# Kernel tuning notes

Measured on AMD Instinct MI355X. Metric: run time of the kernel, lower is better.

## Reference

```python
import jax, jax.numpy as jnp
import numpy as np

D = 64; B = 1024; M = 32; K = 16; L = 8
N_ENT = 200000; N_REL_VOCAB = 65; N_USERS = 100000; NKG = 65536
KG_WEIGHT = 1.0


def _normalize(x, eps=1e-12):
    n = jnp.sqrt(jnp.sum(x * x, axis=-1, keepdims=True))
    return x / jnp.maximum(n, eps)


def _forward(entity_emb, relation_emb, user_emb, gate, W_u_mlp, b_u_mlp, W_re,
             W_agg, b_agg, W_gatt, b_gatt, W_iatt, b_iatt, W_tatt, b_tatt,
             W_ih, W_hh, b_ih, b_hh,
             user_indices, ent_his_self, ent_his_nbr, rel_his,
             ent_pos_self, ent_pos_nbr, rel_pos,
             ent_neg_self, ent_neg_nbr, rel_neg,
             gb_his_self, gb_his_path, gb_pos_self, gb_pos_path,
             gb_neg_self, gb_neg_path, kg_head, kg_rel, kg_tail, kg_tail_neg):

    def gru_last(x):  # x: [N, L, D] -> final hidden [N, D] (PyTorch GRU gate order r,z,n)
        def step(h, xt):
            gi = xt @ W_ih.T + b_ih
            gh = h @ W_hh.T + b_hh
            ir, iz, in_ = jnp.split(gi, 3, axis=-1)
            hr, hz, hn = jnp.split(gh, 3, axis=-1)
            r = jax.nn.sigmoid(ir + hr)
            z = jax.nn.sigmoid(iz + hz)
            n = jnp.tanh(in_ + r * hn)
            return (1 - z) * n + z * h, None
        h0 = jnp.zeros((x.shape[0], D), x.dtype)
        hT, _ = jax.lax.scan(step, h0, jnp.swapaxes(x, 0, 1))
        return hT

    def agg_lc(self_idx, nbr_idx, rel_idx, u_em):
        # self_idx [N,1], nbr_idx/rel_idx [N,K], u_em [N,D]
        self_v = entity_emb[self_idx[:, 0]]                       # [N,D]
        nbr_v = entity_emb[nbr_idx]                               # [N,K,D]
        rel_v = relation_emb[rel_idx]                             # [N,K,D]
        nere = jnp.concatenate([nbr_v, rel_v], -1) @ W_re.T       # [N,K,D]
        u_att = jax.nn.relu(u_em @ W_tatt.T + b_tatt)             # [N,D]
        self1 = jnp.broadcast_to(self_v[:, None, :], nbr_v.shape)
        trans = jnp.tanh(jnp.concatenate([self1, nere], -1) @ W_gatt.T + b_gatt)
        att = jax.nn.softmax(jnp.sum(u_att[:, None, :] * trans, -1), axis=1)  # [N,K]
        new_v = jnp.einsum('nk,nkd->nd', att, nbr_v)
        agg = jnp.tanh(jnp.concatenate([self_v, new_v], -1) @ W_agg.T + b_agg)
        return self_v, _normalize(agg)

    def agg_gb(self_idx, path_idx):
        self_v = entity_emb[self_idx[:, 0]]
        hT = gru_last(entity_emb[path_idx])
        agg = jnp.tanh(jnp.concatenate([self_v, hT], -1) @ W_agg.T + b_agg)
        return _normalize(agg)

    def rs_att(hist, pre):  # hist [B,M,2D], pre [B,2D]
        pre_e = jnp.broadcast_to(pre[:, None, :], hist.shape)
        logits = jnp.tanh(jnp.concatenate([hist, pre_e], -1) @ W_iatt.T + b_iatt)[..., 0]
        att = jax.nn.softmax(logits, axis=1)
        return jnp.einsum('bm,bmd->bd', att, hist)

    user_g = user_emb[user_indices]                               # [B,D]
    g = jax.nn.sigmoid(gate)

    N = B * M
    u_rep = jnp.broadcast_to(user_g[:, None, :], (B, M, D)).reshape(N, D)
    self_hist, his_lc = agg_lc(ent_his_self.reshape(N, 1), ent_his_nbr.reshape(N, K),
                               rel_his.reshape(N, K), u_rep)
    his_gb = agg_gb(gb_his_self.reshape(N, 1), gb_his_path.reshape(N, L))
    item_hist = jnp.concatenate(
        [self_hist.reshape(B, M, D),
         (g * his_lc + (1 - g) * his_gb).reshape(B, M, D)], -1)   # [B,M,2D]

    def item_branch(self_idx, nbr_idx, rel_idx, gb_self, gb_path):
        self_v, lc = agg_lc(self_idx, nbr_idx, rel_idx, user_g)
        gb = agg_gb(gb_self, gb_path)
        item = jnp.concatenate([self_v, g * lc + (1 - g) * gb], -1)  # [B,2D]
        u_lc = rs_att(item_hist, item)                               # [B,2D]
        u = jax.nn.relu(jnp.concatenate([user_g, u_lc], -1) @ W_u_mlp.T + b_u_mlp)
        u = jnp.concatenate([user_g, _normalize(u)], -1)             # [B,2D]
        return jnp.sum(u * item, axis=1)

    pos_score = item_branch(ent_pos_self, ent_pos_nbr, rel_pos, gb_pos_self, gb_pos_path)
    neg_score = item_branch(ent_neg_self, ent_neg_nbr, rel_neg, gb_neg_self, gb_neg_path)
    rs_loss = -jnp.mean(jax.nn.log_sigmoid(pos_score - neg_score))

    head = entity_emb[kg_head]; rel = relation_emb[kg_rel]
    tail = entity_emb[kg_tail]; tail_ne = entity_emb[kg_tail_neg]
    nere = jnp.concatenate([tail, rel], 1) @ W_re.T
    nere_ne = jnp.concatenate([tail_ne, rel], 1) @ W_re.T
    s = jnp.sum((head - nere) ** 2, 1)
    s_ne = jnp.sum((head - nere_ne) ** 2, 1)
    kg_loss = -jnp.mean(jax.nn.log_sigmoid(s_ne - s))

    all_loss = rs_loss + KG_WEIGHT * kg_loss
    return pos_score, neg_score, all_loss


def setup_inputs() -> dict:
    key = jax.random.key(0)
    ks = iter(jax.random.split(key, 48))

    def nrm(shape, scale=0.1):
        return (scale * jax.random.normal(next(ks), shape)).astype(jnp.float32)

    def idx(shape, hi):
        return jax.random.randint(next(ks), shape, 0, hi)

    return dict(
        user_indices=idx((B,), N_USERS),
        ent_his_self=idx((B, M, 1), N_ENT),
        ent_his_nbr=idx((B, M, K), N_ENT),
        rel_his=idx((B, M, K), N_REL_VOCAB),
        ent_pos_self=idx((B, 1), N_ENT),
        ent_pos_nbr=idx((B, K), N_ENT),
        rel_pos=idx((B, K), N_REL_VOCAB),
        ent_neg_self=idx((B, 1), N_ENT),
        ent_neg_nbr=idx((B, K), N_ENT),
        rel_neg=idx((B, K), N_REL_VOCAB),
        gb_his_self=idx((B, M, 1), N_ENT),
        gb_his_path=idx((B, M, L), N_ENT),
        gb_pos_self=idx((B, 1), N_ENT),
        gb_pos_path=idx((B, L), N_ENT),
        gb_neg_self=idx((B, 1), N_ENT),
        gb_neg_path=idx((B, L), N_ENT),
        kg_head=idx((NKG,), N_ENT),
        kg_rel=idx((NKG,), N_REL_VOCAB),
        kg_tail=idx((NKG,), N_ENT),
        kg_tail_neg=idx((NKG,), N_ENT),
        entity_emb=nrm((N_ENT, D)),
        relation_emb=nrm((N_REL_VOCAB, D)),
        user_emb=nrm((N_USERS, D)),
        gate=jnp.zeros((D,), jnp.float32),
        W_u_mlp=nrm((D, 3 * D)), b_u_mlp=jnp.zeros((D,), jnp.float32),
        W_re=nrm((D, 2 * D)),
        W_agg=nrm((D, 2 * D)), b_agg=jnp.zeros((D,), jnp.float32),
        W_gatt=nrm((D, 2 * D)), b_gatt=jnp.zeros((D,), jnp.float32),
        W_iatt=nrm((1, 4 * D)), b_iatt=jnp.zeros((1,), jnp.float32),
        W_tatt=nrm((D, D)), b_tatt=jnp.zeros((D,), jnp.float32),
        W_ih=nrm((3 * D, D)), W_hh=nrm((3 * D, D)),
        b_ih=jnp.zeros((3 * D,), jnp.float32), b_hh=jnp.zeros((3 * D,), jnp.float32),
    )


def reference(user_indices, ent_his_self, ent_his_nbr, rel_his,
              ent_pos_self, ent_pos_nbr, rel_pos,
              ent_neg_self, ent_neg_nbr, rel_neg,
              gb_his_self, gb_his_path, gb_pos_self, gb_pos_path,
              gb_neg_self, gb_neg_path, kg_head, kg_rel, kg_tail, kg_tail_neg,
              entity_emb, relation_emb, user_emb, gate, W_u_mlp, b_u_mlp, W_re,
              W_agg, b_agg, W_gatt, b_gatt, W_iatt, b_iatt, W_tatt, b_tatt,
              W_ih, W_hh, b_ih, b_hh):
    return _forward(entity_emb, relation_emb, user_emb, gate, W_u_mlp, b_u_mlp, W_re,
                    W_agg, b_agg, W_gatt, b_gatt, W_iatt, b_iatt, W_tatt, b_tatt,
                    W_ih, W_hh, b_ih, b_hh,
                    user_indices, ent_his_self, ent_his_nbr, rel_his,
                    ent_pos_self, ent_pos_nbr, rel_pos,
                    ent_neg_self, ent_neg_nbr, rel_neg,
                    gb_his_self, gb_his_path, gb_pos_self, gb_pos_path,
                    gb_neg_self, gb_neg_path, kg_head, kg_rel, kg_tail, kg_tail_neg)
```

## Files before the change

### kernel.cpp

```cpp
#include <hip/hip_runtime.h>

#define DEV __device__ __forceinline__

#define Dd   64
#define Bb   1024
#define Mm   32
#define Kk   16
#define Ll   8
#define NKGk 65536
#define NH   32768
#define ROWS (NH + 2*Bb)

typedef float v2f __attribute__((ext_vector_type(2)));

#define OFF_WTATT   0
#define OFF_WGS     4096
#define OFF_WCOMB   8192
#define OFF_WRE     16384
#define OFF_WAGG    24576
#define OFF_WU      32768
#define OFF_GVEC    45056
#define OFF_USERG   45120
#define OFF_UATT    110656
#define OFF_SELFH   176192
#define OFF_HISLC   2273344
#define OFF_HISGB   4370496
#define OFF_SELFPN  6467648
#define OFF_LCPN    6598720
#define OFF_GBPN    6729792
#define OFF_ULCPN   6860864
#define OFF_KGSUM   7123008
#define OFF_KGS     7123012
#define OFF_WIHP    7123072
#define OFF_WHHP    7135360
#define OFF_WAGP    7147648
#define OFF_RELC    7155840
#define OFF_RELR    7160000

DEV float4 ld4(const float* p){ return *reinterpret_cast<const float4*>(p); }
DEV void st4(float* p, const float4 v){ *reinterpret_cast<float4*>(p) = v; }

DEV float tanh_fast(float x){
  float cx = fminf(15.f, fmaxf(-15.f, x));
  float e = __expf(2.f*cx);
  return __fdividef(e - 1.f, e + 1.f);
}
DEV float sigmoid_fast(float x){ return __fdividef(1.f, 1.f + __expf(-x)); }

#define MVJ(ACC_, WROW_, XS_) { \
  _Pragma("unroll") for (int d4_ = 0; d4_ < 16; ++d4_){ \
    float4 w_ = *(const float4*)((WROW_) + 4*d4_); \
    ACC_[4*d4_+0] += w_.x*(XS_); ACC_[4*d4_+1] += w_.y*(XS_); \
    ACC_[4*d4_+2] += w_.z*(XS_); ACC_[4*d4_+3] += w_.w*(XS_); } }

__global__ void prep1_kernel(const float* __restrict__ W_tatt, const float* __restrict__ W_gatt,
                             const float* __restrict__ W_re, const float* __restrict__ W_agg,
                             const float* __restrict__ W_u, const float* __restrict__ W_ih,
                             const float* __restrict__ W_hh, const float* __restrict__ gate,
                             float* __restrict__ ws)
{
  int g = blockIdx.x*256 + threadIdx.x;
  for (int i = g; i < 4096; i += 8192){
    int d = i >> 6, j = i & 63;
    ws[OFF_WTATT + j*64 + d] = W_tatt[i];
    ws[OFF_WGS   + j*64 + d] = W_gatt[d*128 + j];
  }
  for (int i = g; i < 8192; i += 8192){
    int j = i >> 6, d = i & 63;
    ws[OFF_WRE  + i] = W_re[d*128 + j];
    ws[OFF_WAGG + i] = W_agg[d*128 + j];
    float s = 0.f;
    for (int dp = 0; dp < 64; ++dp) s += W_gatt[d*128 + 64 + dp] * W_re[dp*128 + j];
    ws[OFF_WCOMB + i] = s;
  }
  for (int i = g; i < 12288; i += 8192){
    int j = i >> 6, d = i & 63;
    ws[OFF_WU + i] = W_u[d*192 + j];
  }
  for (int i = g; i < 12288; i += 8192){
    int jc = i / 768, r1 = i - jc*768;
    int ww = r1 / 96,  r2 = r1 - ww*96;
    int jj = r2 / 24,  r3 = r2 - jj*24;
    int gg = r3 >> 3,  oi = r3 & 7;
    int j = jc*4 + jj, o = gg*64 + ww*8 + oi;
    ws[OFF_WIHP + i] = W_ih[o*64 + j];
    ws[OFF_WHHP + i] = W_hh[o*64 + j];
  }
  for (int i = g; i < 8192; i += 8192){
    int jc = i >> 8, r1 = i & 255;
    int ww = r1 >> 5, r2 = r1 & 31;
    int jj = r2 >> 3, oi = r2 & 7;
    ws[OFF_WAGP + i] = W_agg[(ww*8 + oi)*128 + jc*4 + jj];
  }
  if (g < 64) ws[OFF_GVEC + g] = sigmoid_fast(gate[g]);
}

__global__ void prep2_kernel(const float* __restrict__ relation, float* __restrict__ ws)
{
  int i = blockIdx.x*256 + threadIdx.x;
  if (i >= 4160) return;
  int r = i >> 6, d = i & 63;
  const float* re = relation + r*64;
  float s1 = 0.f, s2 = 0.f;
  for (int j = 0; j < 64; ++j){
    s1 += ws[OFF_WCOMB + (64+j)*64 + d] * re[j];
    s2 += ws[OFF_WRE   + (64+j)*64 + d] * re[j];
  }
  ws[OFF_RELC + i] = s1;
  ws[OFF_RELR + i] = s2;
}

__global__ void user_prep_kernel(const int* __restrict__ uidx, const float* __restrict__ user_emb,
                                 const float* __restrict__ b_tatt, float* __restrict__ ws)
{
  int gid = blockIdx.x*256 + threadIdx.x;
  int b = gid >> 6, lane = gid & 63;
  long ui = uidx[b];
  float ugd = user_emb[ui*64 + lane];
  ws[OFF_USERG + b*64 + lane] = ugd;
  const float* WtT = ws + OFF_WTATT;
  float acc = b_tatt[lane];
  for (int j = 0; j < 64; ++j) acc += WtT[j*64 + lane] * __shfl(ugd, j);
  ws[OFF_UATT + b*64 + lane] = fmaxf(acc, 0.f);
}

#define GACC(AR_, AZ_, AN_, WP_, XS_) { \
  v2f xx_; xx_.x = (XS_); xx_.y = (XS_); \
  AR_[0] += (*(const v2f*)((WP_)+ 0))*xx_; AR_[1] += (*(const v2f*)((WP_)+ 2))*xx_; \
  AR_[2] += (*(const v2f*)((WP_)+ 4))*xx_; AR_[3] += (*(const v2f*)((WP_)+ 6))*xx_; \
  AZ_[0] += (*(const v2f*)((WP_)+ 8))*xx_; AZ_[1] += (*(const v2f*)((WP_)+10))*xx_; \
  AZ_[2] += (*(const v2f*)((WP_)+12))*xx_; AZ_[3] += (*(const v2f*)((WP_)+14))*xx_; \
  AN_[0] += (*(const v2f*)((WP_)+16))*xx_; AN_[1] += (*(const v2f*)((WP_)+18))*xx_; \
  AN_[2] += (*(const v2f*)((WP_)+20))*xx_; AN_[3] += (*(const v2f*)((WP_)+22))*xx_; }

#define AGACC(AG_, WP_, XS_) { \
  v2f xx_; xx_.x = (XS_); xx_.y = (XS_); \
  AG_[0] += (*(const v2f*)((WP_)+0))*xx_; AG_[1] += (*(const v2f*)((WP_)+2))*xx_; \
  AG_[2] += (*(const v2f*)((WP_)+4))*xx_; AG_[3] += (*(const v2f*)((WP_)+6))*xx_; }

__global__ __launch_bounds__(512, 4) void fused_kernel(
  const int* __restrict__ ghS, const int* __restrict__ ghP,
  const int* __restrict__ gpS, const int* __restrict__ gpP,
  const int* __restrict__ gnS, const int* __restrict__ gnP,
  const float* __restrict__ b_ih, const float* __restrict__ b_hh,
  const float* __restrict__ WIHP, const float* __restrict__ WHHP,
  const float* __restrict__ WAGP,
  float* __restrict__ outHis, float* __restrict__ outPN,
  const int* __restrict__ ahS, const int* __restrict__ ahN, const int* __restrict__ ahR,
  const int* __restrict__ apS, const int* __restrict__ apN, const int* __restrict__ apR,
  const int* __restrict__ anS, const int* __restrict__ anN, const int* __restrict__ anR,
  const float* __restrict__ b_gatt, const float* __restrict__ b_agg,
  const float* __restrict__ entity, float* __restrict__ ws)
{
  __shared__ float SH[8320];
  int tid = threadIdx.x;
  int bid = blockIdx.x;
  int rep = bid / 3, pos = bid - rep*3;

  if (pos == 0){
    float (*hb)[65] = (float(*)[65])SH;
    float (*xb)[65] = (float(*)[65])(SH + 4160);
    int w = __builtin_amdgcn_readfirstlane(tid >> 6);
    int lane = tid & 63;
    int rbase = rep*64;
    const int *sIv, *pIv; float* aO; int nb0;
    if (rbase < NH)          { sIv=ghS; pIv=ghP; aO=outHis;       nb0=rbase; }
    else if (rbase < NH+Bb)  { sIv=gpS; pIv=gpP; aO=outPN;        nb0=rbase-NH; }
    else                     { sIv=gnS; pIv=gnP; aO=outPN+65536;  nb0=rbase-NH-Bb; }
    int o0 = w*8;
    int nrow = nb0 + lane;

    int pt = pIv[nrow*8];
    int pt_next = pIv[nrow*8 + 1];
    {
      const float* ex = entity + (long)pt*64 + o0;
      float4 xa0 = ld4(ex), xc0 = ld4(ex + 4);
      st4(&xb[lane][o0], xa0);
      st4(&xb[lane][o0+4], xc0);
    }
    __syncthreads();

    #pragma unroll 1
    for (int t = 0; t < 8; ++t){
      float4 xa = {0,0,0,0}, xc = {0,0,0,0};
      if (t < 7){
        const float* ex = entity + (long)pt_next*64 + o0;
        xa = ld4(ex); xc = ld4(ex + 4);
        if (t < 6) pt_next = pIv[nrow*8 + t + 2];
      }
      v2f ar[4], az[4], ah[4];
      #pragma unroll
      for (int p = 0; p < 4; ++p){
        ar[p].x = b_ih[o0+2*p]      + b_hh[o0+2*p];
        ar[p].y = b_ih[o0+2*p+1]    + b_hh[o0+2*p+1];
        az[p].x = b_ih[64+o0+2*p]   + b_hh[64+o0+2*p];
        az[p].y = b_ih[64+o0+2*p+1] + b_hh[64+o0+2*p+1];
        ah[p].x = b_hh[128+o0+2*p];   ah[p].y = b_hh[128+o0+2*p+1];
      }
      if (t){
        #pragma unroll 2
        for (int jc = 0; jc < 16; ++jc){
          const float* wp = WHHP + (jc*8 + w)*96;
          float4 h4 = ld4(&hb[lane][4*jc]);
          GACC(ar, az, ah, wp,      h4.x);
          GACC(ar, az, ah, wp + 24, h4.y);
          GACC(ar, az, ah, wp + 48, h4.z);
          GACC(ar, az, ah, wp + 72, h4.w);
        }
      }
      v2f an[4];
      #pragma unroll
      for (int p = 0; p < 4; ++p){ an[p].x = b_ih[128+o0+2*p]; an[p].y = b_ih[128+o0+2*p+1]; }
      #pragma unroll 2
      for (int jc = 0; jc < 16; ++jc){
        const float* wp = WIHP + (jc*8 + w)*96;
        float4 x4 = ld4(&xb[lane][4*jc]);
        GACC(ar, az, an, wp,      x4.x);
        GACC(ar, az, an, wp + 24, x4.y);
        GACC(ar, az, an, wp + 48, x4.z);
        GACC(ar, az, an, wp + 72, x4.w);
      }
      float hp[8] = {0,0,0,0,0,0,0,0};
      if (t){
        float4 hv0 = ld4(&hb[lane][o0]); float4 hv1 = ld4(&hb[lane][o0+4]);
        hp[0]=hv0.x; hp[1]=hv0.y; hp[2]=hv0.z; hp[3]=hv0.w;
        hp[4]=hv1.x; hp[5]=hv1.y; hp[6]=hv1.z; hp[7]=hv1.w;
      }
      float hn[8];
      #pragma unroll
      for (int p = 0; p < 4; ++p){
        float r0 = sigmoid_fast(ar[p].x), r1 = sigmoid_fast(ar[p].y);
        float z0 = sigmoid_fast(az[p].x), z1 = sigmoid_fast(az[p].y);
        float n0 = tanh_fast(an[p].x + r0*ah[p].x);
        float n1 = tanh_fast(an[p].y + r1*ah[p].y);
        hn[2*p]   = (1.f - z0)*n0 + z0*hp[2*p];
        hn[2*p+1] = (1.f - z1)*n1 + z1*hp[2*p+1];
      }
      __syncthreads();
      float4 s0 = {hn[0],hn[1],hn[2],hn[3]}, s1 = {hn[4],hn[5],hn[6],hn[7]};
      st4(&hb[lane][o0], s0);
      st4(&hb[lane][o0+4], s1);
      if (t < 7){
        st4(&xb[lane][o0], xa);
        st4(&xb[lane][o0+4], xc);
      }
      __syncthreads();
    }

    long si = sIv[nrow];
    const float* es = entity + si*64 + o0;
    float4 aa = ld4(es), cc = ld4(es + 4);
    v2f ag[4];
    #pragma unroll
    for (int p = 0; p < 4; ++p){ ag[p].x = b_agg[o0+2*p]; ag[p].y = b_agg[o0+2*p+1]; }
    #pragma unroll 2
    for (int jc = 0; jc < 16; ++jc){
      const float* wp = WAGP + ((16+jc)*8 + w)*32;
      float4 h4 = ld4(&hb[lane][4*jc]);
      AGACC(ag, wp,      h4.x);
      AGACC(ag, wp + 8,  h4.y);
      AGACC(ag, wp + 16, h4.z);
      AGACC(ag, wp + 24, h4.w);
    }
    st4(&xb[lane][o0], aa);
    st4(&xb[lane][o0+4], cc);
    __syncthreads();
    #pragma unroll 2
    for (int jc = 0; jc < 16; ++jc){
      const float* wp = WAGP + (jc*8 + w)*32;
      float4 x4 = ld4(&xb[lane][4*jc]);
      AGACC(ag, wp,      x4.x);
      AGACC(ag, wp + 8,  x4.y);
      AGACC(ag, wp + 16, x4.z);
      AGACC(ag, wp + 24, x4.w);
    }
    {
      float4 s0 = {tanh_fast(ag[0].x), tanh_fast(ag[0].y), tanh_fast(ag[1].x), tanh_fast(ag[1].y)};
      float4 s1 = {tanh_fast(ag[2].x), tanh_fast(ag[2].y), tanh_fast(ag[3].x), tanh_fast(ag[3].y)};
      st4(&hb[lane][o0], s0);
      st4(&hb[lane][o0+4], s1);
    }
    __syncthreads();
    int q = tid & 7, r = tid >> 3;
    float4 v0 = ld4(&hb[r][q*8]);
    float4 v1 = ld4(&hb[r][q*8+4]);
    float ss = v0.x*v0.x + v0.y*v0.y + v0.z*v0.z + v0.w*v0.w
             + v1.x*v1.x + v1.y*v1.y + v1.z*v1.z + v1.w*v1.w;
    ss += __shfl_xor(ss, 1); ss += __shfl_xor(ss, 2); ss += __shfl_xor(ss, 4);
    float rn = __fdividef(1.f, fmaxf(sqrtf(ss), 1e-12f));
    int n2 = nb0 + r;
    float4 o4a = {v0.x*rn, v0.y*rn, v0.z*rn, v0.w*rn};
    float4 o4b = {v1.x*rn, v1.y*rn, v1.z*rn, v1.w*rn};
    st4(aO + (long)n2*64 + q*8,     o4a);
    st4(aO + (long)n2*64 + q*8 + 4, o4b);
    return;
  }

  float* WL = SH;
  int ablk = rep*2 + (pos - 1);
  int tid2 = tid & 255;
  int sub  = tid >> 8;
  int k = tid2 & 15, rl = tid2 >> 4;
  int rbase = ablk*32;
  const int *sI, *nI, *rI; float *sO, *aO; int nb0, uhis;
  if (rbase < NH)          { sI=ahS; nI=ahN; rI=ahR; sO=ws+OFF_SELFH;        aO=ws+OFF_HISLC;       nb0=rbase;        uhis=1; }
  else if (rbase < NH+Bb)  { sI=apS; nI=apN; rI=apR; sO=ws+OFF_SELFPN;       aO=ws+OFF_LCPN;       nb0=rbase-NH;     uhis=0; }
  else                     { sI=anS; nI=anN; rI=anR; sO=ws+OFF_SELFPN+65536; aO=ws+OFF_LCPN+65536; nb0=rbase-NH-Bb;  uhis=0; }
  int n = nb0 + sub*16 + rl;
  int urow = uhis ? (n >> 5) : n;

  for (int i = tid; i < 1024; i += 512){
    st4(&WL[4*i],        ld4(ws + OFF_WCOMB + 4*i));
    st4(&WL[4096 + 4*i], ld4(ws + OFF_WGS   + 4*i));
  }

  const float* es = entity + (long)sI[n]*64;
  long nbI = nI[n*16 + k], rlI = rI[n*16 + k];
  const float* en = entity + nbI*64;

  float acc[64];
  {
    const float* rt = ws + OFF_RELC + rlI*64;
    #pragma unroll
    for (int j4 = 0; j4 < 16; ++j4){
      float4 v = ld4(rt + 4*j4);
      acc[4*j4+0] = v.x; acc[4*j4+1] = v.y; acc[4*j4+2] = v.z; acc[4*j4+3] = v.w;
    }
  }
  __syncthreads();

  float4 sc4 = ld4(b_gatt + k*4);
  #pragma unroll 2
  for (int j4 = 0; j4 < 16; ++j4){
    float4 s4 = ld4(es + 4*j4);
    float4 w0 = *(const float4*)&WL[4096 + (4*j4+0)*64 + k*4];
    float4 w1 = *(const float4*)&WL[4096 + (4*j4+1)*64 + k*4];
    float4 w2 = *(const float4*)&WL[4096 + (4*j4+2)*64 + k*4];
    float4 w3 = *(const float4*)&WL[4096 + (4*j4+3)*64 + k*4];
    sc4.x += w0.x*s4.x + w1.x*s4.y + w2.x*s4.z + w3.x*s4.w;
    sc4.y += w0.y*s4.x + w1.y*s4.y + w2.y*s4.z + w3.y*s4.w;
    sc4.z += w0.z*s4.x + w1.z*s4.y + w2.z*s4.z + w3.z*s4.w;
    sc4.w += w0.w*s4.x + w1.w*s4.y + w2.w*s4.z + w3.w*s4.w;
  }
  st4(sO + (long)n*64 + k*4, ld4(es + k*4));

  {
    float4 x4 = ld4(en);
    #pragma unroll 2
    for (int j4 = 0; j4 < 16; ++j4){
      float4 xn = ld4(en + 4*((j4+1) & 15));
      MVJ(acc, &WL[(4*j4+0)*64], x4.x);
      MVJ(acc, &WL[(4*j4+1)*64], x4.y);
      MVJ(acc, &WL[(4*j4+2)*64], x4.z);
      MVJ(acc, &WL[(4*j4+3)*64], x4.w);
      x4 = xn;
    }
  }

  int gl = (tid & 63) & 48;
  const float* up = ws + OFF_UATT + (long)urow*64;
  float lg = 0.f;
  #pragma unroll
  for (int j4 = 0; j4 < 16; ++j4){
    float4 u4 = ld4(up + 4*j4);
    float s0 = __shfl(sc4.x, gl + j4);
    float s1 = __shfl(sc4.y, gl + j4);
    float s2 = __shfl(sc4.z, gl + j4);
    float s3 = __shfl(sc4.w, gl + j4);
    lg += u4.x*tanh_fast(acc[4*j4+0] + s0);
    lg += u4.y*tanh_fast(acc[4*j4+1] + s1);
    lg += u4.z*tanh_fast(acc[4*j4+2] + s2);
    lg += u4.w*tanh_fast(acc[4*j4+3] + s3);
  }
  float mx = lg;
  mx = fmaxf(mx, __shfl_xor(mx, 1)); mx = fmaxf(mx, __shfl_xor(mx, 2));
  mx = fmaxf(mx, __shfl_xor(mx, 4)); mx = fmaxf(mx, __shfl_xor(mx, 8));
  float e = __expf(lg - mx);
  float se = e;
  se += __shfl_xor(se, 1); se += __shfl_xor(se, 2);
  se += __shfl_xor(se, 4); se += __shfl_xor(se, 8);
  float att = __fdividef(e, se);

  __syncthreads();
  for (int i = tid; i < 2048; i += 512)
    st4(&WL[4*i], ld4(ws + OFF_WAGG + 4*i));
  __syncthreads();

  float4 a4 = ld4(b_agg + k*4);
  #pragma unroll 2
  for (int j4 = 0; j4 < 16; ++j4){
    float4 s4 = ld4(es + 4*j4);
    float4 w0 = *(const float4*)&WL[(4*j4+0)*64 + k*4];
    float4 w1 = *(const float4*)&WL[(4*j4+1)*64 + k*4];
    float4 w2 = *(const float4*)&WL[(4*j4+2)*64 + k*4];
    float4 w3 = *(const float4*)&WL[(4*j4+3)*64 + k*4];
    a4.x += w0.x*s4.x + w1.x*s4.y + w2.x*s4.z + w3.x*s4.w;
    a4.y += w0.y*s4.x + w1.y*s4.y + w2.y*s4.z + w3.y*s4.w;
    a4.z += w0.z*s4.x + w1.z*s4.y + w2.z*s4.z + w3.z*s4.w;
    a4.w += w0.w*s4.x + w1.w*s4.y + w2.w*s4.z + w3.w*s4.w;
  }
  #pragma unroll 2
  for (int j4 = 0; j4 < 16; ++j4){
    float4 x4 = ld4(en + 4*j4);
    float xs[4] = {x4.x, x4.y, x4.z, x4.w};
    #pragma unroll
    for (int jj = 0; jj < 4; ++jj){
      float v = att * xs[jj];
      v += __shfl_xor(v, 1); v += __shfl_xor(v, 2);
      v += __shfl_xor(v, 4); v += __shfl_xor(v, 8);
      float4 wv = *(const float4*)&WL[(64 + 4*j4 + jj)*64 + k*4];
      a4.x += wv.x*v; a4.y += wv.y*v; a4.z += wv.z*v; a4.w += wv.w*v;
    }
  }
  float t0 = tanh_fast(a4.x), t1 = tanh_fast(a4.y), t2 = tanh_fast(a4.z), t3 = tanh_fast(a4.w);
  float ss = t0*t0 + t1*t1 + t2*t2 + t3*t3;
  ss += __shfl_xor(ss, 1); ss += __shfl_xor(ss, 2);
  ss += __shfl_xor(ss, 4); ss += __shfl_xor(ss, 8);
  float rn = __fdividef(1.f, fmaxf(sqrtf(ss), 1e-12f));
  float4 o4; o4.x = t0*rn; o4.y = t1*rn; o4.z = t2*rn; o4.w = t3*rn;
  st4(aO + (long)n*64 + k*4, o4);
}

__global__ __launch_bounds__(512, 4) void fused2_kernel(
  const int* __restrict__ kh, const int* __restrict__ kr,
  const int* __restrict__ kt, const int* __restrict__ ktn,
  const float* __restrict__ W_iatt, const float* __restrict__ b_iatt,
  const float* __restrict__ b_u,
  const float* __restrict__ entity, const float* __restrict__ relation,
  float* __restrict__ ws, float* __restrict__ out)
{
  __shared__ float WL[4096];
  int tid = threadIdx.x;
  int bid = blockIdx.x;
  int type = bid & 1, rep = bid >> 1;

  if (type == 0){
    int idx = rep*512 + tid;
    int br = idx >> 16, r = idx & 65535;
    const int* tailI = br ? ktn : kt;
    for (int i = tid; i < 1024; i += 512)
      st4(&WL[4*i], ld4(ws + OFF_WRE + 4*i));

    long rel = kr[r];
    const float* et = entity + (long)tailI[r]*64;
    float acc[64];
    {
      const float* rt = ws + OFF_RELR + rel*64;
      #pragma unroll
      for (int j4 = 0; j4 < 16; ++j4){
        float4 v = ld4(rt + 4*j4);
        acc[4*j4+0] = v.x; acc[4*j4+1] = v.y; acc[4*j4+2] = v.z; acc[4*j4+3] = v.w;
      }
    }
    __syncthreads();
    {
      float4 x4 = ld4(et);
      #pragma unroll 2
      for (int j4 = 0; j4 < 16; ++j4){
        float4 xn = ld4(et + 4*((j4+1) & 15));
        MVJ(acc, &WL[(4*j4+0)*64], x4.x);
        MVJ(acc, &WL[(4*j4+1)*64], x4.y);
        MVJ(acc, &WL[(4*j4+2)*64], x4.z);
        MVJ(acc, &WL[(4*j4+3)*64], x4.w);
        x4 = xn;
      }
    }
    const float* eh = entity + (long)kh[r]*64;
    float s = 0.f;
    #pragma unroll
    for (int j4 = 0; j4 < 16; ++j4){
      float4 h4 = ld4(eh + 4*j4);
      float d0 = h4.x - acc[4*j4+0], d1 = h4.y - acc[4*j4+1];
      float d2 = h4.z - acc[4*j4+2], d3 = h4.w - acc[4*j4+3];
      s += d0*d0 + d1*d1 + d2*d2 + d3*d3;
    }
    ws[OFF_KGS + br*65536 + r] = s;
    return;
  }

  int gw = rep*8 + (tid >> 6), lane = tid & 63;
  int b = gw >> 1, br = gw & 1;
  const float* selfB = ws + OFF_SELFPN + br*65536 + b*64;
  const float* lcB   = ws + OFF_LCPN   + br*65536 + b*64;
  const float* gbB   = ws + OFF_GBPN   + br*65536 + b*64;
  const float* gvec  = ws + OFF_GVEC;
  const float* selfH = ws + OFF_SELFH;
  const float* hisLC = ws + OFF_HISLC;
  const float* hisGB = ws + OFF_HISGB;

  float gd = gvec[lane];
  float ugd = ws[OFF_USERG + b*64 + lane];
  float sv = selfB[lane], lcv = lcB[lane], gbv = gbB[lane];
  float gated = gd*lcv + (1.f - gd)*gbv;
  float part = W_iatt[128+lane]*sv + W_iatt[192+lane]*gated;
  #pragma unroll
  for (int m2 = 1; m2 < 64; m2 <<= 1) part += __shfl_xor(part, m2);
  float itemdot = part + b_iatt[0];

  int m = lane & 31, half = lane >> 5;
  long nrow = (long)(b*32 + m)*64;
  float sh = 0.f;
  if (half == 0){
    for (int j4 = 0; j4 < 16; ++j4){
      float4 h4 = ld4(selfH + nrow + 4*j4);
      float4 w4 = ld4(W_iatt + 4*j4);
      sh += w4.x*h4.x + w4.y*h4.y + w4.z*h4.z + w4.w*h4.w;
    }
  } else {
    for (int j4 = 0; j4 < 16; ++j4){
      float4 l4 = ld4(hisLC + nrow + 4*j4);
      float4 g4 = ld4(hisGB + nrow + 4*j4);
      float4 gg = ld4(gvec + 4*j4);
      float4 w4 = ld4(W_iatt + 64 + 4*j4);
      sh += w4.x*(gg.x*l4.x + (1.f-gg.x)*g4.x);
      sh += w4.y*(gg.y*l4.y + (1.f-gg.y)*g4.y);
      sh += w4.z*(gg.z*l4.z + (1.f-gg.z)*g4.z);
      sh += w4.w*(gg.w*l4.w + (1.f-gg.w)*g4.w);
    }
  }
  sh += __shfl_xor(sh, 32);
  float logit = tanh_fast(sh + itemdot);
  float mxv = logit;
  #pragma unroll
  for (int m2 = 1; m2 < 32; m2 <<= 1) mxv = fmaxf(mxv, __shfl_xor(mxv, m2));
  float e = __expf(logit - mxv);
  float se = e;
  #pragma unroll
  for (int m2 = 1; m2 < 32; m2 <<= 1) se += __shfl_xor(se, m2);
  float att = __fdividef(e, se);

  float u1 = 0.f, u2 = 0.f;
  for (int mm = 0; mm < 32; ++mm){
    float a = __shfl(att, mm);
    long nr = (long)(b*32 + mm)*64;
    float x1 = selfH[nr + lane];
    float x2 = gd*hisLC[nr + lane] + (1.f - gd)*hisGB[nr + lane];
    u1 += a*x1; u2 += a*x2;
  }

  const float* WuT = ws + OFF_WU;
  float acc = b_u[lane];
  for (int j = 0; j < 64; ++j) acc += WuT[j*64 + lane]        * __shfl(ugd, j);
  for (int j = 0; j < 64; ++j) acc += WuT[(64 + j)*64 + lane] * __shfl(u1, j);
  for (int j = 0; j < 64; ++j) acc += WuT[(128 + j)*64 + lane]* __shfl(u2, j);
  float uo = fmaxf(acc, 0.f);
  float ssv = uo*uo;
  #pragma unroll
  for (int m2 = 1; m2 < 64; m2 <<= 1) ssv += __shfl_xor(ssv, m2);
  float rn = __fdividef(1.f, fmaxf(sqrtf(ssv), 1e-12f));
  float nuo = uo*rn;
  float p = ugd*sv + nuo*gated;
  #pragma unroll
  for (int m2 = 1; m2 < 64; m2 <<= 1) p += __shfl_xor(p, m2);
  if (lane == 0) out[br*1024 + b] = p;
}

__global__ void kg_reduce_kernel(float* __restrict__ ws)
{
  int r = blockIdx.x*256 + threadIdx.x;
  float s  = ws[OFF_KGS + r];
  float sn = ws[OFF_KGS + 65536 + r];
  float dif = sn - s;
  float ls = fminf(dif, 0.f) - __logf(1.f + __expf(-fabsf(dif)));
  #pragma unroll
  for (int m2 = 1; m2 < 64; m2 <<= 1) ls += __shfl_xor(ls, m2);
  if ((threadIdx.x & 63) == 0) atomicAdd(ws + OFF_KGSUM, ls);
}

__global__ void loss_kernel(const float* __restrict__ ws, float* __restrict__ out)
{
  __shared__ float red[16];
  int t = threadIdx.x;
  float ps = out[t], ns_ = out[1024 + t];
  float dif = ps - ns_;
  float v = fminf(dif, 0.f) - __logf(1.f + __expf(-fabsf(dif)));
  #pragma unroll
  for (int m2 = 1; m2 < 64; m2 <<= 1) v += __shfl_xor(v, m2);
  if ((t & 63) == 0) red[t >> 6] = v;
  __syncthreads();
  if (t == 0){
    float s = 0.f;
    for (int i = 0; i < 16; ++i) s += red[i];
    float rs = -s * (1.f/1024.f);
    float kg = -ws[OFF_KGSUM] * (1.f/65536.f);
    out[2048] = rs + kg;
  }
}

extern "C" void kernel_launch(void* const* d_in, const int* in_sizes, int n_in,
                              void* d_out, int out_size, void* d_ws, size_t ws_size,
                              hipStream_t stream)
{
  const int* user_indices = (const int*)d_in[0];
  const int* ent_his_self = (const int*)d_in[1];
  const int* ent_his_nbr  = (const int*)d_in[2];
  const int* rel_his      = (const int*)d_in[3];
  const int* ent_pos_self = (const int*)d_in[4];
  const int* ent_pos_nbr  = (const int*)d_in[5];
  const int* rel_pos      = (const int*)d_in[6];
  const int* ent_neg_self = (const int*)d_in[7];
  const int* ent_neg_nbr  = (const int*)d_in[8];
  const int* rel_neg      = (const int*)d_in[9];
  const int* gb_his_self  = (const int*)d_in[10];
  const int* gb_his_path  = (const int*)d_in[11];
  const int* gb_pos_self  = (const int*)d_in[12];
  const int* gb_pos_path  = (const int*)d_in[13];
  const int* gb_neg_self  = (const int*)d_in[14];
  const int* gb_neg_path  = (const int*)d_in[15];
  const int* kg_head      = (const int*)d_in[16];
  const int* kg_rel       = (const int*)d_in[17];
  const int* kg_tail      = (const int*)d_in[18];
  const int* kg_tail_neg  = (const int*)d_in[19];
  const float* entity_emb   = (const float*)d_in[20];
  const float* relation_emb = (const float*)d_in[21];
  const float* user_emb     = (const float*)d_in[22];
  const float* gate         = (const float*)d_in[23];
  const float* W_u_mlp      = (const float*)d_in[24];
  const float* b_u_mlp      = (const float*)d_in[25];
  const float* W_re         = (const float*)d_in[26];
  const float* W_agg        = (const float*)d_in[27];
  const float* b_agg        = (const float*)d_in[28];
  const float* W_gatt       = (const float*)d_in[29];
  const float* b_gatt       = (const float*)d_in[30];
  const float* W_iatt       = (const float*)d_in[31];
  const float* b_iatt       = (const float*)d_in[32];
  const float* W_tatt       = (const float*)d_in[33];
  const float* b_tatt       = (const float*)d_in[34];
  const float* W_ih         = (const float*)d_in[35];
  const float* W_hh         = (const float*)d_in[36];
  const float* b_ih         = (const float*)d_in[37];
  const float* b_hh         = (const float*)d_in[38];
  float* ws  = (float*)d_ws;
  float* out = (float*)d_out;

  (void)hipMemsetAsync(ws + OFF_KGSUM, 0, sizeof(float), stream);
  prep1_kernel<<<32, 256, 0, stream>>>(W_tatt, W_gatt, W_re, W_agg, W_u_mlp, W_ih, W_hh, gate, ws);
  prep2_kernel<<<17, 256, 0, stream>>>(relation_emb, ws);
  user_prep_kernel<<<256, 256, 0, stream>>>(user_indices, user_emb, b_tatt, ws);
  fused_kernel<<<1632, 512, 0, stream>>>(
      gb_his_self, gb_his_path, gb_pos_self, gb_pos_path,
      gb_neg_self, gb_neg_path,
      b_ih, b_hh,
      ws + OFF_WIHP, ws + OFF_WHHP, ws + OFF_WAGP,
      ws + OFF_HISGB, ws + OFF_GBPN,
      ent_his_self, ent_his_nbr, rel_his,
      ent_pos_self, ent_pos_nbr, rel_pos,
      ent_neg_self, ent_neg_nbr, rel_neg,
      b_gatt, b_agg,
      entity_emb, ws);
  fused2_kernel<<<512, 512, 0, stream>>>(
      kg_head, kg_rel, kg_tail, kg_tail_neg,
      W_iatt, b_iatt, b_u_mlp,
      entity_emb, relation_emb, ws, out);
  kg_reduce_kernel<<<256, 256, 0, stream>>>(ws);
  loss_kernel<<<1, 1024, 0, stream>>>(ws, out);
}
```

Measured before the change: 647.4 us.

## Use packed float2 FMA in matvecs and schedule GRU blocks first

Rewrites the 64-wide matrix-vector accumulations in the aggregation and KG-score paths to use two-element float vectors, so the compiler can emit packed FP32 FMA instructions (v_pk_fma_f32) and roughly halve the FMA instruction count. It also changes the block layout of the fused kernel: instead of interleaving one GRU block with two aggregation blocks, all GRU blocks now come first and aggregation blocks follow, which changes load balance and the tail of the launch. Packed math may change register allocation, and the new block order may expose the longer GRU blocks differently.

```diff
diff --git a/kernel.cpp b/kernel.cpp
--- a/kernel.cpp
+++ b/kernel.cpp
@@ -10,6 +10,7 @@
 #define NKGk 65536
 #define NH   32768
 #define ROWS (NH + 2*Bb)
+#define NGRU (ROWS/64)
 
 typedef float v2f __attribute__((ext_vector_type(2)));
 
@@ -47,11 +48,11 @@
 }
 DEV float sigmoid_fast(float x){ return __fdividef(1.f, 1.f + __expf(-x)); }
 
-#define MVJ(ACC_, WROW_, XS_) { \
+#define MVJ2(ACC2_, WROW_, XX_) { \
   _Pragma("unroll") for (int d4_ = 0; d4_ < 16; ++d4_){ \
     float4 w_ = *(const float4*)((WROW_) + 4*d4_); \
-    ACC_[4*d4_+0] += w_.x*(XS_); ACC_[4*d4_+1] += w_.y*(XS_); \
-    ACC_[4*d4_+2] += w_.z*(XS_); ACC_[4*d4_+3] += w_.w*(XS_); } }
+    ACC2_[2*d4_]   += (v2f){w_.x, w_.y}*(XX_); \
+    ACC2_[2*d4_+1] += (v2f){w_.z, w_.w}*(XX_); } }
 
 __global__ void prep1_kernel(const float* __restrict__ W_tatt, const float* __restrict__ W_gatt,
                              const float* __restrict__ W_re, const float* __restrict__ W_agg,
@@ -155,9 +156,9 @@
   __shared__ float SH[8320];
   int tid = threadIdx.x;
   int bid = blockIdx.x;
-  int rep = bid / 3, pos = bid - rep*3;
-
-  if (pos == 0){
+
+  if (bid < NGRU){
+    int rep = bid;
     float (*hb)[65] = (float(*)[65])SH;
     float (*xb)[65] = (float(*)[65])(SH + 4160);
     int w = __builtin_amdgcn_readfirstlane(tid >> 6);
@@ -297,7 +298,7 @@
   }
 
   float* WL = SH;
-  int ablk = rep*2 + (pos - 1);
+  int ablk = bid - NGRU;
   int tid2 = tid & 255;
   int sub  = tid >> 8;
   int k = tid2 & 15, rl = tid2 >> 4;
@@ -318,13 +319,14 @@
   long nbI = nI[n*16 + k], rlI = rI[n*16 + k];
   const float* en = entity + nbI*64;
 
-  float acc[64];
+  v2f acc2[32];
   {
     const float* rt = ws + OFF_RELC + rlI*64;
     #pragma unroll
     for (int j4 = 0; j4 < 16; ++j4){
       float4 v = ld4(rt + 4*j4);
-      acc[4*j4+0] = v.x; acc[4*j4+1] = v.y; acc[4*j4+2] = v.z; acc[4*j4+3] = v.w;
+      acc2[2*j4]   = (v2f){v.x, v.y};
+      acc2[2*j4+1] = (v2f){v.z, v.w};
     }
   }
   __syncthreads();
@@ -349,10 +351,14 @@
     #pragma unroll 2
     for (int j4 = 0; j4 < 16; ++j4){
       float4 xn = ld4(en + 4*((j4+1) & 15));
-      MVJ(acc, &WL[(4*j4+0)*64], x4.x);
-      MVJ(acc, &WL[(4*j4+1)*64], x4.y);
-      MVJ(acc, &WL[(4*j4+2)*64], x4.z);
-      MVJ(acc, &WL[(4*j4+3)*64], x4.w);
+      v2f xx0; xx0.x = x4.x; xx0.y = x4.x;
+      MVJ2(acc2, &WL[(4*j4+0)*64], xx0);
+      v2f xx1; xx1.x = x4.y; xx1.y = x4.y;
+      MVJ2(acc2, &WL[(4*j4+1)*64], xx1);
+      v2f xx2; xx2.x = x4.z; xx2.y = x4.z;
+      MVJ2(acc2, &WL[(4*j4+2)*64], xx2);
+      v2f xx3; xx3.x = x4.w; xx3.y = x4.w;
+      MVJ2(acc2, &WL[(4*j4+3)*64], xx3);
       x4 = xn;
     }
   }
@@ -367,10 +373,10 @@
     float s1 = __shfl(sc4.y, gl + j4);
     float s2 = __shfl(sc4.z, gl + j4);
     float s3 = __shfl(sc4.w, gl + j4);
-    lg += u4.x*tanh_fast(acc[4*j4+0] + s0);
-    lg += u4.y*tanh_fast(acc[4*j4+1] + s1);
-    lg += u4.z*tanh_fast(acc[4*j4+2] + s2);
-    lg += u4.w*tanh_fast(acc[4*j4+3] + s3);
+    lg += u4.x*tanh_fast(acc2[2*j4].x   + s0);
+    lg += u4.y*tanh_fast(acc2[2*j4].y   + s1);
+    lg += u4.z*tanh_fast(acc2[2*j4+1].x + s2);
+    lg += u4.w*tanh_fast(acc2[2*j4+1].y + s3);
   }
   float mx = lg;
   mx = fmaxf(mx, __shfl_xor(mx, 1)); mx = fmaxf(mx, __shfl_xor(mx, 2));
@@ -443,13 +449,14 @@
 
     long rel = kr[r];
     const float* et = entity + (long)tailI[r]*64;
-    float acc[64];
+    v2f acc2[32];
     {
       const float* rt = ws + OFF_RELR + rel*64;
       #pragma unroll
       for (int j4 = 0; j4 < 16; ++j4){
         float4 v = ld4(rt + 4*j4);
-        acc[4*j4+0] = v.x; acc[4*j4+1] = v.y; acc[4*j4+2] = v.z; acc[4*j4+3] = v.w;
+        acc2[2*j4]   = (v2f){v.x, v.y};
+        acc2[2*j4+1] = (v2f){v.z, v.w};
       }
     }
     __syncthreads();
@@ -458,10 +465,14 @@
       #pragma unroll 2
       for (int j4 = 0; j4 < 16; ++j4){
         float4 xn = ld4(et + 4*((j4+1) & 15));
-        MVJ(acc, &WL[(4*j4+0)*64], x4.x);
-        MVJ(acc, &WL[(4*j4+1)*64], x4.y);
-        MVJ(acc, &WL[(4*j4+2)*64], x4.z);
-        MVJ(acc, &WL[(4*j4+3)*64], x4.w);
+        v2f xx0; xx0.x = x4.x; xx0.y = x4.x;
+        MVJ2(acc2, &WL[(4*j4+0)*64], xx0);
+        v2f xx1; xx1.x = x4.y; xx1.y = x4.y;
+        MVJ2(acc2, &WL[(4*j4+1)*64], xx1);
+        v2f xx2; xx2.x = x4.z; xx2.y = x4.z;
+        MVJ2(acc2, &WL[(4*j4+2)*64], xx2);
+        v2f xx3; xx3.x = x4.w; xx3.y = x4.w;
+        MVJ2(acc2, &WL[(4*j4+3)*64], xx3);
         x4 = xn;
       }
     }
@@ -470,8 +481,8 @@
     #pragma unroll
     for (int j4 = 0; j4 < 16; ++j4){
       float4 h4 = ld4(eh + 4*j4);
-      float d0 = h4.x - acc[4*j4+0], d1 = h4.y - acc[4*j4+1];
-      float d2 = h4.z - acc[4*j4+2], d3 = h4.w - acc[4*j4+3];
+      float d0 = h4.x - acc2[2*j4].x,   d1 = h4.y - acc2[2*j4].y;
+      float d2 = h4.z - acc2[2*j4+1].x, d3 = h4.w - acc2[2*j4+1].y;
       s += d0*d0 + d1*d1 + d2*d2 + d3*d3;
     }
     ws[OFF_KGS + br*65536 + r] = s;
```

New measurement: 598.3 us. -7.6%, faster.
